# Kernel tuning notes

Hardware: AMD Instinct MI355X
Metric: run time of the kernel (lower is better)

Reference implementation:

```python
import jax, jax.numpy as jnp
import numpy as np

N, TOT, D, DK, C, NH = 64, 8192, 64, 32, 16, 8
L = TOT // C  # 512


def setup_inputs() -> dict:
    key = jax.random.key(0)
    kx, kq, kk = jax.random.split(key, 3)
    x = jax.random.normal(kx, (N, TOT, D), dtype=jnp.float32)
    # match torch reset_parameters: uniform(-stdv, stdv)
    stdv_q = 1.0 / np.sqrt(C)
    stdv_k = 1.0 / np.sqrt(D)
    W_q = jax.random.uniform(kq, (NH, C, D, DK), dtype=jnp.float32,
                             minval=-stdv_q, maxval=stdv_q)
    W_k = jax.random.uniform(kk, (NH, D, DK), dtype=jnp.float32,
                             minval=-stdv_k, maxval=stdv_k)
    return {"x": x, "W_q": W_q, "W_k": W_k}


def reference(x, W_q, W_k):
    nH, C_, D_, Dk = W_q.shape
    n = x.shape[0]
    xr = x.reshape(n, -1, C_, D_)               # (n, L, C, D)
    # Q[n,h,l,t] = sum_{c,d} x[n,l,c,d] * W_q[h,c,d,t]
    Q = jnp.einsum('nlcd,hcdt->nhlt', xr, W_q)
    # Fuse K with Q contraction to avoid the (n,h,l,C,Dk) intermediate:
    # QK[n,h,l,c] = sum_{d,t} x[n,l,c,d] W_k[h,d,t] Q[n,h,l,t]
    A = jnp.einsum('hdt,nhlt->nhld', W_k, Q)    # (n, nH, L, D)
    QK = jnp.einsum('nlcd,nhld->nhlc', xr, A) / jnp.sqrt(jnp.float32(Dk))
    score = jax.nn.softmax(QK, axis=-1)         # softmax over channel dim C
    attn = jnp.einsum('nhlc,nlcd->nhld', score, xr)
    # concat heads on last axis (head order preserved)
    out = jnp.transpose(attn, (0, 2, 1, 3)).reshape(n, xr.shape[1], nH * D_)
    return out
```

## Files before the change

kernel.cpp:

```cpp
#include <hip/hip_runtime.h>
#include <stdint.h>


typedef __attribute__((ext_vector_type(4))) float  f32x4;
typedef __attribute__((ext_vector_type(8))) __bf16 bf16x8;
typedef __attribute__((ext_vector_type(4))) unsigned int u32x4;

#define P_TOT 32768
#define NCOL  512

__device__ __align__(16) unsigned short g_Mpre[524288];
__device__ __align__(16) unsigned short g_A[(size_t)P_TOT * NCOL];

static __device__ __forceinline__ unsigned short f2bf(float f) {
  unsigned int u = __float_as_uint(f);
  u += 0x7FFFu + ((u >> 16) & 1u);
  return (unsigned short)(u >> 16);
}
static __device__ __forceinline__ unsigned int pk2(float lo, float hi) {
  return ((unsigned int)f2bf(hi) << 16) | (unsigned int)f2bf(lo);
}
static __device__ __forceinline__ float bflo(unsigned int w) { return __uint_as_float(w << 16); }
static __device__ __forceinline__ float bfhi(unsigned int w) { return __uint_as_float(w & 0xFFFF0000u); }

__global__ void __launch_bounds__(256)
fold_wqk(const float* __restrict__ Wq, const float* __restrict__ Wk) {
  int idx  = (blockIdx.x << 8) + threadIdx.x;
  int j    = idx & 7;
  int lane = (idx >> 3) & 63;
  int ctg  = (idx >> 9) & 31;
  int skk  = idx >> 14;
  int k    = (skk << 5) + ((lane >> 4) << 3) + j;
  int col  = (ctg << 4) + (lane & 15);
  int h    = col >> 6;
  int d    = col & 63;
  const float* wq = Wq + ((size_t)h << 15) + ((size_t)k << 5);
  const float* wk = Wk + ((size_t)h << 11) + ((size_t)d << 5);
  float acc = 0.f;
#pragma unroll
  for (int t = 0; t < 32; ++t) acc = fmaf(wq[t], wk[t], acc);
  g_Mpre[idx] = f2bf(acc * 0.17677669529663687f);
}

__global__ void __launch_bounds__(256, 2)
gemm_A(const float* __restrict__ x) {
  extern __shared__ char smem[];
  const int tid  = threadIdx.x;
  const int lane = tid & 63;
  const int wave = tid >> 6;
  const int wm   = wave >> 1;
  const int wn   = wave & 1;

  const int bid = blockIdx.x;
  const int swz = ((bid & 7) << 7) + (bid >> 3);
  const int bn  = swz & 3;
  const int pm  = swz >> 2;
  const float* xb = x + ((size_t)pm << 17);

  const int srow = tid >> 1;
  const int skh  = tid & 1;

  f32x4 acc[4][4];
#pragma unroll
  for (int mt = 0; mt < 4; ++mt)
#pragma unroll
    for (int nt = 0; nt < 4; ++nt)
#pragma unroll
      for (int r = 0; r < 4; ++r) acc[mt][nt][r] = 0.f;

  {
    const float* src = xb + (size_t)srow * 1024 + (skh << 5);
#pragma unroll
    for (int q = 0; q < 4; ++q) {
      f32x4 a = ((const f32x4*)src)[q * 2];
      f32x4 b = ((const f32x4*)src)[q * 2 + 1];
      u32x4 w; w[0] = pk2(a[0], a[1]); w[1] = pk2(a[2], a[3]);
               w[2] = pk2(b[0], b[1]); w[3] = pk2(b[2], b[3]);
      unsigned off = ((unsigned)srow << 7) + ((unsigned)skh << 6) + ((unsigned)q << 4);
      off ^= ((unsigned)srow & 7u) << 4;
      *(u32x4*)(smem + off) = w;
    }
#pragma unroll
    for (int i = 0; i < 4; ++i) {
      int g  = tid + (i << 8);
      int kk = g >> 9, ct8 = (g >> 6) & 7, lp = g & 63;
      size_t sidx = ((size_t)((kk << 5) + (bn << 3) + ct8) << 9) + ((size_t)lp << 3);
      *(u32x4*)(smem + 32768 + (g << 4)) = *(const u32x4*)(g_Mpre + sidx);
    }
  }
  __syncthreads();

  int buf = 0;
  for (int s = 0; s < 16; ++s) {
    f32x4 xv[8]; u32x4 mv[4];
    const bool more = (s + 1) < 16;
    if (more) {
      const float* src = xb + (size_t)srow * 1024 + ((s + 1) << 6) + (skh << 5);
#pragma unroll
      for (int q = 0; q < 8; ++q) xv[q] = ((const f32x4*)src)[q];
#pragma unroll
      for (int i = 0; i < 4; ++i) {
        int g  = tid + (i << 8);
        int kk = g >> 9, ct8 = (g >> 6) & 7, lp = g & 63;
        size_t sidx = ((size_t)((((s + 1) * 2 + kk) << 5) + (bn << 3) + ct8) << 9) + ((size_t)lp << 3);
        mv[i] = *(const u32x4*)(g_Mpre + sidx);
      }
    }
    {
      const char* xl = smem + (buf << 14);
      const char* ml = smem + 32768 + (buf << 14);
#pragma unroll
      for (int kk = 0; kk < 2; ++kk) {
        bf16x8 a[4], b[4];
#pragma unroll
        for (int mt = 0; mt < 4; ++mt) {
          int row = (wm << 6) + (mt << 4) + (lane & 15);
          unsigned off = ((unsigned)row << 7) + ((unsigned)kk << 6) + (((unsigned)lane >> 4) << 4);
          off ^= ((unsigned)row & 7u) << 4;
          a[mt] = *(const bf16x8*)(xl + off);
        }
#pragma unroll
        for (int nt = 0; nt < 4; ++nt)
          b[nt] = *(const bf16x8*)(ml + (kk << 13) + (((((wn << 2) + nt) << 6) + lane) << 4));
#pragma unroll
        for (int mt = 0; mt < 4; ++mt)
#pragma unroll
          for (int nt = 0; nt < 4; ++nt)
            acc[mt][nt] = __builtin_amdgcn_mfma_f32_16x16x32_bf16(a[mt], b[nt], acc[mt][nt], 0, 0, 0);
      }
    }
    if (more) {
      char* xd = smem + ((buf ^ 1) << 14);
#pragma unroll
      for (int q = 0; q < 4; ++q) {
        u32x4 w; w[0] = pk2(xv[q*2][0], xv[q*2][1]); w[1] = pk2(xv[q*2][2], xv[q*2][3]);
                 w[2] = pk2(xv[q*2+1][0], xv[q*2+1][1]); w[3] = pk2(xv[q*2+1][2], xv[q*2+1][3]);
        unsigned off = ((unsigned)srow << 7) + ((unsigned)skh << 6) + ((unsigned)q << 4);
        off ^= ((unsigned)srow & 7u) << 4;
        *(u32x4*)(xd + off) = w;
      }
      char* md = smem + 32768 + ((buf ^ 1) << 14);
#pragma unroll
      for (int i = 0; i < 4; ++i)
        *(u32x4*)(md + ((tid + (i << 8)) << 4)) = mv[i];
    }
    __syncthreads();
    buf ^= 1;
  }

#pragma unroll
  for (int mt = 0; mt < 4; ++mt)
#pragma unroll
    for (int nt = 0; nt < 4; ++nt)
#pragma unroll
      for (int r = 0; r < 4; ++r) {
        size_t row = ((size_t)pm << 7) + (wm << 6) + (mt << 4) + ((lane >> 4) << 2) + r;
        int    col = (bn << 7) + (wn << 6) + (nt << 4) + (lane & 15);
        g_A[(row << 9) + col] = f2bf(acc[mt][nt][r]);
      }
}

__global__ void __launch_bounds__(512)
attn_ep(const float* __restrict__ x, float* __restrict__ out) {
  __shared__ char xs[32768];
  const int tid  = threadIdx.x;
  const int pos0 = blockIdx.x << 4;

  {
    const float* src = x + ((size_t)pos0 << 10);
#pragma unroll
    for (int i = 0; i < 4; ++i) {
      int g = tid + (i << 9);
      f32x4 a = *(const f32x4*)(src + ((size_t)g << 3));
      f32x4 b = *(const f32x4*)(src + ((size_t)g << 3) + 4);
      u32x4 w; w[0] = pk2(a[0], a[1]); w[1] = pk2(a[2], a[3]);
               w[2] = pk2(b[0], b[1]); w[3] = pk2(b[2], b[3]);
      unsigned off = (unsigned)g << 4;
      off ^= (((unsigned)g >> 7) & 1u) << 4;
      *(u32x4*)(xs + off) = w;
    }
  }
  __syncthreads();

  const int q   = tid & 3;
  const int h   = (tid >> 2) & 7;
  const int pos = tid >> 5;
  const unsigned pswz = ((unsigned)pos & 1u) << 4;

  float av[16];
  {
    const unsigned short* ap = g_A + (((size_t)(pos0 + pos)) << 9) + (h << 6) + (q << 4);
    u32x4 w0 = *(const u32x4*)ap;
    u32x4 w1 = *(const u32x4*)(ap + 8);
#pragma unroll
    for (int i = 0; i < 4; ++i) {
      av[2*i]     = bflo(w0[i]);  av[2*i + 1] = bfhi(w0[i]);
      av[8 + 2*i] = bflo(w1[i]);  av[9 + 2*i] = bfhi(w1[i]);
    }
  }

  const unsigned xbase = ((unsigned)pos << 11) + ((unsigned)q << 5);

  float qk[16];
#pragma unroll
  for (int c = 0; c < 16; ++c) {
    unsigned cb = xbase + ((unsigned)c << 7);
    u32x4 v0 = *(const u32x4*)(xs + (cb ^ pswz));
    u32x4 v1 = *(const u32x4*)(xs + ((cb + 16u) ^ pswz));
    float dt = 0.f;
#pragma unroll
    for (int i = 0; i < 4; ++i) {
      dt = fmaf(bflo(v0[i]), av[2*i],     dt);
      dt = fmaf(bfhi(v0[i]), av[2*i + 1], dt);
      dt = fmaf(bflo(v1[i]), av[8 + 2*i], dt);
      dt = fmaf(bfhi(v1[i]), av[9 + 2*i], dt);
    }
    dt += __shfl_xor(dt, 1, 64);
    dt += __shfl_xor(dt, 2, 64);
    qk[c] = dt;
  }

  float mx = qk[0];
#pragma unroll
  for (int c = 1; c < 16; ++c) mx = fmaxf(mx, qk[c]);
  float sum = 0.f;
#pragma unroll
  for (int c = 0; c < 16; ++c) { qk[c] = __expf(qk[c] - mx); sum += qk[c]; }
  const float inv = 1.0f / sum;

  float o[16];
#pragma unroll
  for (int i = 0; i < 16; ++i) o[i] = 0.f;
#pragma unroll
  for (int c = 0; c < 16; ++c) {
    float wc = qk[c] * inv;
    unsigned cb = xbase + ((unsigned)c << 7);
    u32x4 v0 = *(const u32x4*)(xs + (cb ^ pswz));
    u32x4 v1 = *(const u32x4*)(xs + ((cb + 16u) ^ pswz));
#pragma unroll
    for (int i = 0; i < 4; ++i) {
      o[2*i]     = fmaf(bflo(v0[i]), wc, o[2*i]);
      o[2*i + 1] = fmaf(bfhi(v0[i]), wc, o[2*i + 1]);
      o[8 + 2*i] = fmaf(bflo(v1[i]), wc, o[8 + 2*i]);
      o[9 + 2*i] = fmaf(bfhi(v1[i]), wc, o[9 + 2*i]);
    }
  }

  float* op = out + (((size_t)(pos0 + pos)) << 9) + (h << 6) + (q << 4);
#pragma unroll
  for (int j = 0; j < 4; ++j)
    *(f32x4*)(op + (j << 2)) = *(f32x4*)&o[j * 4];
}

extern "C" void kernel_launch(void* const* d_in, const int* in_sizes, int n_in,
                              void* d_out, int out_size, void* d_ws, size_t ws_size,
                              hipStream_t stream) {
  (void)in_sizes; (void)n_in; (void)d_ws; (void)ws_size; (void)out_size;
  const float* x  = (const float*)d_in[0];
  const float* Wq = (const float*)d_in[1];
  const float* Wk = (const float*)d_in[2];
  float* out = (float*)d_out;

  (void)hipFuncSetAttribute((const void*)gemm_A,
                            hipFuncAttributeMaxDynamicSharedMemorySize, 65536);

  fold_wqk<<<2048, 256, 0, stream>>>(Wq, Wk);
  gemm_A<<<1024, 256, 65536, stream>>>(x);
  attn_ep<<<P_TOT / 16, 512, 0, stream>>>(x, out);
}
```

Before: 395.6 us.

## Pre-convert x to bf16 once and stream tiles via global_load_lds

Adds a cvt_x kernel that converts x to a bf16 global buffer once. gemm_A and attn_ep then read that buffer directly into LDS with global_load_lds DMA instead of each loading fp32 x and converting it in registers. gemm_A is restructured to 32 half-size K steps with smaller double buffers (32KB static LDS instead of 64KB dynamic). The aim is to halve x read traffic in both consumers and shorten the load/convert path. In exchange it adds an extra kernel launch plus a full bf16 write and read of x, and drops the LDS swizzle in attn_ep, which may cause bank conflicts.

After: 369.9 us. 1.07x faster.

```diff
diff --git a/kernel.cpp b/kernel.cpp
--- a/kernel.cpp
+++ b/kernel.cpp
@@ -7,10 +7,10 @@
 typedef __attribute__((ext_vector_type(4))) unsigned int u32x4;
 
 #define P_TOT 32768
-#define NCOL  512
 
 __device__ __align__(16) unsigned short g_Mpre[524288];
-__device__ __align__(16) unsigned short g_A[(size_t)P_TOT * NCOL];
+__device__ __align__(16) unsigned short g_A[(size_t)P_TOT * 512];
+__device__ __align__(16) unsigned short g_xbf[(size_t)P_TOT * 1024];
 
 static __device__ __forceinline__ unsigned short f2bf(float f) {
   unsigned int u = __float_as_uint(f);
@@ -22,6 +22,26 @@
 }
 static __device__ __forceinline__ float bflo(unsigned int w) { return __uint_as_float(w << 16); }
 static __device__ __forceinline__ float bfhi(unsigned int w) { return __uint_as_float(w & 0xFFFF0000u); }
+
+typedef __attribute__((address_space(3))) void lds_void;
+typedef const __attribute__((address_space(1))) void gbl_void;
+static __device__ __forceinline__ void glds16(const void* g, void* l) {
+  __builtin_amdgcn_global_load_lds((gbl_void*)(uintptr_t)g,
+                                   (lds_void*)(uint32_t)(uintptr_t)l, 16, 0, 0);
+}
+
+__global__ void __launch_bounds__(256)
+cvt_x(const float* __restrict__ x) {
+  int g = (blockIdx.x << 10) + threadIdx.x;
+#pragma unroll
+  for (int i = 0; i < 4; ++i, g += 256) {
+    const f32x4* src = (const f32x4*)(x + ((size_t)g << 3));
+    f32x4 a = src[0], b = src[1];
+    u32x4 w; w[0] = pk2(a[0], a[1]); w[1] = pk2(a[2], a[3]);
+             w[2] = pk2(b[0], b[1]); w[3] = pk2(b[2], b[3]);
+    *(u32x4*)(g_xbf + ((size_t)g << 3)) = w;
+  }
+}
 
 __global__ void __launch_bounds__(256)
 fold_wqk(const float* __restrict__ Wq, const float* __restrict__ Wk) {
@@ -42,9 +62,10 @@
   g_Mpre[idx] = f2bf(acc * 0.17677669529663687f);
 }
 
-__global__ void __launch_bounds__(256, 2)
-gemm_A(const float* __restrict__ x) {
-  extern __shared__ char smem[];
+__global__ void __launch_bounds__(256)
+gemm_A() {
+  __shared__ __align__(16) char xs[2][8192];
+  __shared__ __align__(16) char ms[2][8192];
   const int tid  = threadIdx.x;
   const int lane = tid & 63;
   const int wave = tid >> 6;
@@ -55,10 +76,23 @@
   const int swz = ((bid & 7) << 7) + (bid >> 3);
   const int bn  = swz & 3;
   const int pm  = swz >> 2;
-  const float* xb = x + ((size_t)pm << 17);
-
-  const int srow = tid >> 1;
-  const int skh  = tid & 1;
+
+  const int d0 = tid, d1 = 256 + tid;
+  const int xr0 = d0 >> 2, xc0 = (d0 & 3) ^ ((d0 >> 3) & 3);
+  const int xr1 = d1 >> 2, xc1 = (d1 & 3) ^ ((d1 >> 3) & 3);
+  const char* xg0 = (const char*)g_xbf + (((size_t)(pm * 128 + xr0)) << 11) + (xc0 << 4);
+  const char* xg1 = (const char*)g_xbf + (((size_t)(pm * 128 + xr1)) << 11) + (xc1 << 4);
+  const char* mg  = (const char*)g_Mpre + ((size_t)bn << 13) + (tid << 4);
+
+  char* xd0 = &xs[0][0] + (wave << 10);
+  char* xd1 = &xs[0][0] + 4096 + (wave << 10);
+  char* md0 = &ms[0][0] + (wave << 10);
+  char* md1 = &ms[0][0] + 4096 + (wave << 10);
+
+  const int l4    = lane & 15;
+  const int aslot = ((lane >> 4) ^ ((lane >> 1) & 3)) << 4;
+  const int abase = (((wm << 6) + l4) << 6);
+  const int bbase = (((wn << 8) + lane) << 4);
 
   f32x4 acc[4][4];
 #pragma unroll
@@ -68,85 +102,39 @@
 #pragma unroll
       for (int r = 0; r < 4; ++r) acc[mt][nt][r] = 0.f;
 
-  {
-    const float* src = xb + (size_t)srow * 1024 + (skh << 5);
-#pragma unroll
-    for (int q = 0; q < 4; ++q) {
-      f32x4 a = ((const f32x4*)src)[q * 2];
-      f32x4 b = ((const f32x4*)src)[q * 2 + 1];
-      u32x4 w; w[0] = pk2(a[0], a[1]); w[1] = pk2(a[2], a[3]);
-               w[2] = pk2(b[0], b[1]); w[3] = pk2(b[2], b[3]);
-      unsigned off = ((unsigned)srow << 7) + ((unsigned)skh << 6) + ((unsigned)q << 4);
-      off ^= ((unsigned)srow & 7u) << 4;
-      *(u32x4*)(smem + off) = w;
-    }
-#pragma unroll
-    for (int i = 0; i < 4; ++i) {
-      int g  = tid + (i << 8);
-      int kk = g >> 9, ct8 = (g >> 6) & 7, lp = g & 63;
-      size_t sidx = ((size_t)((kk << 5) + (bn << 3) + ct8) << 9) + ((size_t)lp << 3);
-      *(u32x4*)(smem + 32768 + (g << 4)) = *(const u32x4*)(g_Mpre + sidx);
-    }
-  }
+#define STAGE(buf, s) do {                                        \
+    size_t xo = (size_t)(s) << 6;                                 \
+    glds16(xg0 + xo, xd0 + ((buf) << 13));                        \
+    glds16(xg1 + xo, xd1 + ((buf) << 13));                        \
+    const char* mc = mg + ((size_t)(s) << 15);                    \
+    glds16(mc,        md0 + ((buf) << 13));                       \
+    glds16(mc + 4096, md1 + ((buf) << 13));                       \
+  } while (0)
+
+  STAGE(0, 0);
   __syncthreads();
 
-  int buf = 0;
-  for (int s = 0; s < 16; ++s) {
-    f32x4 xv[8]; u32x4 mv[4];
-    const bool more = (s + 1) < 16;
-    if (more) {
-      const float* src = xb + (size_t)srow * 1024 + ((s + 1) << 6) + (skh << 5);
-#pragma unroll
-      for (int q = 0; q < 8; ++q) xv[q] = ((const f32x4*)src)[q];
-#pragma unroll
-      for (int i = 0; i < 4; ++i) {
-        int g  = tid + (i << 8);
-        int kk = g >> 9, ct8 = (g >> 6) & 7, lp = g & 63;
-        size_t sidx = ((size_t)((((s + 1) * 2 + kk) << 5) + (bn << 3) + ct8) << 9) + ((size_t)lp << 3);
-        mv[i] = *(const u32x4*)(g_Mpre + sidx);
-      }
-    }
-    {
-      const char* xl = smem + (buf << 14);
-      const char* ml = smem + 32768 + (buf << 14);
-#pragma unroll
-      for (int kk = 0; kk < 2; ++kk) {
-        bf16x8 a[4], b[4];
-#pragma unroll
-        for (int mt = 0; mt < 4; ++mt) {
-          int row = (wm << 6) + (mt << 4) + (lane & 15);
-          unsigned off = ((unsigned)row << 7) + ((unsigned)kk << 6) + (((unsigned)lane >> 4) << 4);
-          off ^= ((unsigned)row & 7u) << 4;
-          a[mt] = *(const bf16x8*)(xl + off);
-        }
-#pragma unroll
-        for (int nt = 0; nt < 4; ++nt)
-          b[nt] = *(const bf16x8*)(ml + (kk << 13) + (((((wn << 2) + nt) << 6) + lane) << 4));
-#pragma unroll
-        for (int mt = 0; mt < 4; ++mt)
-#pragma unroll
-          for (int nt = 0; nt < 4; ++nt)
-            acc[mt][nt] = __builtin_amdgcn_mfma_f32_16x16x32_bf16(a[mt], b[nt], acc[mt][nt], 0, 0, 0);
-      }
-    }
-    if (more) {
-      char* xd = smem + ((buf ^ 1) << 14);
-#pragma unroll
-      for (int q = 0; q < 4; ++q) {
-        u32x4 w; w[0] = pk2(xv[q*2][0], xv[q*2][1]); w[1] = pk2(xv[q*2][2], xv[q*2][3]);
-                 w[2] = pk2(xv[q*2+1][0], xv[q*2+1][1]); w[3] = pk2(xv[q*2+1][2], xv[q*2+1][3]);
-        unsigned off = ((unsigned)srow << 7) + ((unsigned)skh << 6) + ((unsigned)q << 4);
-        off ^= ((unsigned)srow & 7u) << 4;
-        *(u32x4*)(xd + off) = w;
-      }
-      char* md = smem + 32768 + ((buf ^ 1) << 14);
-#pragma unroll
-      for (int i = 0; i < 4; ++i)
-        *(u32x4*)(md + ((tid + (i << 8)) << 4)) = mv[i];
-    }
+#pragma unroll 2
+  for (int s = 0; s < 32; ++s) {
+    const int cb = s & 1;
+    if (s + 1 < 32) STAGE(cb ^ 1, s + 1);
+    const char* xb = &xs[cb][0];
+    const char* mb = &ms[cb][0];
+    bf16x8 a[4], b[4];
+#pragma unroll
+    for (int mt = 0; mt < 4; ++mt)
+      a[mt] = *(const bf16x8*)(xb + abase + (mt << 10) + aslot);
+#pragma unroll
+    for (int nt = 0; nt < 4; ++nt)
+      b[nt] = *(const bf16x8*)(mb + bbase + (nt << 10));
+#pragma unroll
+    for (int mt = 0; mt < 4; ++mt)
+#pragma unroll
+      for (int nt = 0; nt < 4; ++nt)
+        acc[mt][nt] = __builtin_amdgcn_mfma_f32_16x16x32_bf16(a[mt], b[nt], acc[mt][nt], 0, 0, 0);
     __syncthreads();
-    buf ^= 1;
-  }
+  }
+#undef STAGE
 
 #pragma unroll
   for (int mt = 0; mt < 4; ++mt)
@@ -161,52 +149,40 @@
 }
 
 __global__ void __launch_bounds__(512)
-attn_ep(const float* __restrict__ x, float* __restrict__ out) {
-  __shared__ char xs[32768];
+attn_ep(float* __restrict__ out) {
+  __shared__ __align__(16) char xsl[32768];
   const int tid  = threadIdx.x;
+  const int wave = tid >> 6;
   const int pos0 = blockIdx.x << 4;
 
-  {
-    const float* src = x + ((size_t)pos0 << 10);
-#pragma unroll
-    for (int i = 0; i < 4; ++i) {
-      int g = tid + (i << 9);
-      f32x4 a = *(const f32x4*)(src + ((size_t)g << 3));
-      f32x4 b = *(const f32x4*)(src + ((size_t)g << 3) + 4);
-      u32x4 w; w[0] = pk2(a[0], a[1]); w[1] = pk2(a[2], a[3]);
-               w[2] = pk2(b[0], b[1]); w[3] = pk2(b[2], b[3]);
-      unsigned off = (unsigned)g << 4;
-      off ^= (((unsigned)g >> 7) & 1u) << 4;
-      *(u32x4*)(xs + off) = w;
-    }
-  }
-  __syncthreads();
+  const char* xg = (const char*)g_xbf + ((size_t)pos0 << 11) + (tid << 4);
+#pragma unroll
+  for (int i = 0; i < 4; ++i)
+    glds16(xg + (i << 13), &xsl[0] + (i << 13) + (wave << 10));
 
   const int q   = tid & 3;
   const int h   = (tid >> 2) & 7;
   const int pos = tid >> 5;
-  const unsigned pswz = ((unsigned)pos & 1u) << 4;
+
+  const unsigned short* ap = g_A + (((size_t)(pos0 + pos)) << 9) + (h << 6) + (q << 4);
+  u32x4 w0 = *(const u32x4*)ap;
+  u32x4 w1 = *(const u32x4*)(ap + 8);
+  __syncthreads();
 
   float av[16];
-  {
-    const unsigned short* ap = g_A + (((size_t)(pos0 + pos)) << 9) + (h << 6) + (q << 4);
-    u32x4 w0 = *(const u32x4*)ap;
-    u32x4 w1 = *(const u32x4*)(ap + 8);
-#pragma unroll
-    for (int i = 0; i < 4; ++i) {
-      av[2*i]     = bflo(w0[i]);  av[2*i + 1] = bfhi(w0[i]);
-      av[8 + 2*i] = bflo(w1[i]);  av[9 + 2*i] = bfhi(w1[i]);
-    }
-  }
-
-  const unsigned xbase = ((unsigned)pos << 11) + ((unsigned)q << 5);
+#pragma unroll
+  for (int i = 0; i < 4; ++i) {
+    av[2*i]     = bflo(w0[i]);  av[2*i + 1] = bfhi(w0[i]);
+    av[8 + 2*i] = bflo(w1[i]);  av[9 + 2*i] = bfhi(w1[i]);
+  }
+
+  const char* xb = &xsl[0] + ((unsigned)pos << 11) + ((unsigned)q << 5);
 
   float qk[16];
 #pragma unroll
   for (int c = 0; c < 16; ++c) {
-    unsigned cb = xbase + ((unsigned)c << 7);
-    u32x4 v0 = *(const u32x4*)(xs + (cb ^ pswz));
-    u32x4 v1 = *(const u32x4*)(xs + ((cb + 16u) ^ pswz));
+    u32x4 v0 = *(const u32x4*)(xb + (c << 7));
+    u32x4 v1 = *(const u32x4*)(xb + (c << 7) + 16);
     float dt = 0.f;
 #pragma unroll
     for (int i = 0; i < 4; ++i) {
@@ -234,9 +210,8 @@
 #pragma unroll
   for (int c = 0; c < 16; ++c) {
     float wc = qk[c] * inv;
-    unsigned cb = xbase + ((unsigned)c << 7);
-    u32x4 v0 = *(const u32x4*)(xs + (cb ^ pswz));
-    u32x4 v1 = *(const u32x4*)(xs + ((cb + 16u) ^ pswz));
+    u32x4 v0 = *(const u32x4*)(xb + (c << 7));
+    u32x4 v1 = *(const u32x4*)(xb + (c << 7) + 16);
 #pragma unroll
     for (int i = 0; i < 4; ++i) {
       o[2*i]     = fmaf(bflo(v0[i]), wc, o[2*i]);
@@ -261,10 +236,8 @@
   const float* Wk = (const float*)d_in[2];
   float* out = (float*)d_out;
 
-  (void)hipFuncSetAttribute((const void*)gemm_A,
-                            hipFuncAttributeMaxDynamicSharedMemorySize, 65536);
-
+  cvt_x   <<<4096, 256, 0, stream>>>(x);
   fold_wqk<<<2048, 256, 0, stream>>>(Wq, Wk);
-  gemm_A<<<1024, 256, 65536, stream>>>(x);
-  attn_ep<<<P_TOT / 16, 512, 0, stream>>>(x, out);
-}
+  gemm_A  <<<1024, 256, 0, stream>>>();
+  attn_ep <<<P_TOT / 16, 512, 0, stream>>>(out);
+}
```
